# Kernel optimization log

Measured on AMD Instinct MI355X. Metric: run time of the kernel, lower is better.

The kernel has to match this reference:

```python
import jax, jax.numpy as jnp
import numpy as np
from jax import lax

LOW_T = 25.0    # int(0.1 * 255)
HIGH_T = 76.0   # int(0.3 * 255)
HYST_ITERS = 64 # cap on hysteresis propagation sweeps
TG22 = 0.4142135623730951  # tan(22.5 deg)
TG67 = 2.414213562373095   # tan(67.5 deg)

SOBEL_X = jnp.array([[-1., 0., 1.], [-2., 0., 2.], [-1., 0., 1.]], dtype=jnp.float32)
SOBEL_Y = jnp.array([[-1., -2., -1.], [0., 0., 0.], [1., 2., 1.]], dtype=jnp.float32)


def _conv3(x, k):
    # x: [B,H,W]; reflect-101 border like cv2.Sobel default
    xp = jnp.pad(x, ((0, 0), (1, 1), (1, 1)), mode='reflect')
    return lax.conv_general_dilated(xp[:, None], k[None, None], (1, 1), 'VALID')[:, 0]


def _dilate3x3(m):
    # 3x3 max-pool (8-connected dilation); m is nonnegative float 0/1
    return lax.reduce_window(m, jnp.float32(0.0), lax.max, (1, 3, 3), (1, 1, 1), 'SAME')


def canny_edge(image, low, high):
    """Batched Canny. image: [B,C,H,W] in [0,1] -> edges [B,1,H,W] in {0,1}."""
    image = lax.stop_gradient(image)  # mirrors .cpu().detach().numpy()
    B, C, H, W = image.shape
    if C == 3:
        gray = 0.299 * image[:, 0] + 0.587 * image[:, 1] + 0.114 * image[:, 2]
    else:
        gray = image[:, 0]
    # (img*255).astype(np.uint8) == floor toward zero for values in [0,1]
    g = jnp.clip(jnp.floor(gray * 255.0), 0.0, 255.0)

    gx = _conv3(g, SOBEL_X)
    gy = _conv3(g, SOBEL_Y)
    mag = jnp.abs(gx) + jnp.abs(gy)  # cv2 default L2gradient=False -> L1 magnitude

    # --- non-maximum suppression (OpenCV-style direction quantization) ---
    mp = jnp.pad(mag, ((0, 0), (1, 1), (1, 1)))

    def sh(dy, dx):
        return mp[:, 1 + dy:1 + dy + H, 1 + dx:1 + dx + W]

    ax, ay = jnp.abs(gx), jnp.abs(gy)
    horiz = ay <= TG22 * ax              # gradient ~horizontal: compare L/R
    vert = ay >= TG67 * ax               # gradient ~vertical: compare U/D
    diag = ~(horiz | vert)
    same_sign = (gx * gy) >= 0
    d1 = diag & same_sign                # 45 deg diagonal

    keep_h = (mag > sh(0, -1)) & (mag >= sh(0, 1))
    keep_v = (mag > sh(-1, 0)) & (mag >= sh(1, 0))
    keep_d1 = (mag > sh(-1, -1)) & (mag >= sh(1, 1))
    keep_d2 = (mag > sh(-1, 1)) & (mag >= sh(1, -1))
    keep = jnp.where(horiz, keep_h,
           jnp.where(vert, keep_v,
           jnp.where(d1, keep_d1, keep_d2)))
    nms = jnp.where(keep, mag, 0.0)

    # --- double threshold + hysteresis (iterative 8-connected propagation) ---
    weak = (nms > low).astype(jnp.float32)
    strong = (nms > high).astype(jnp.float32)

    def cond(state):
        cur, prev, i = state
        return jnp.logical_and(i < HYST_ITERS, jnp.any(cur != prev))

    def body(state):
        cur, prev, i = state
        new = jnp.minimum(_dilate3x3(cur), weak)          # grow strong into weak
        new = jnp.maximum(new, strong)
        return new, cur, i + 1

    edges, _, _ = lax.while_loop(cond, body, (strong, -jnp.ones_like(strong), 0))
    return edges[:, None]  # [B,1,H,W]


def reference(image_A, image_B):
    image_A = jnp.where(image_A.max() > 1, image_A / 2.0, image_A)
    image_B = jnp.where(image_B.max() > 1, image_B / 2.0, image_B)
    edges_A = canny_edge(image_A, LOW_T, HIGH_T)
    edges_B = canny_edge(image_B, LOW_T, HIGH_T)
    diff = edges_A - edges_B
    return jnp.sqrt(jnp.sum(diff * diff))  # Frobenius norm over all elements


def setup_inputs() -> dict:
    key = jax.random.key(0)
    kA, kB = jax.random.split(key)
    image_A = jax.random.uniform(kA, (32, 3, 512, 512), dtype=jnp.float32)
    image_B = jax.random.uniform(kB, (32, 3, 512, 512), dtype=jnp.float32)
    return {"image_A": image_A, "image_B": image_B}
```

## Files before the change

### kernel.cpp

```cpp
#include <hip/hip_runtime.h>
#include <cstdint>

#define IMG_H 512
#define IMG_W 512
#define WPR 8

typedef unsigned long long u64;

__global__ __launch_bounds__(256) void canny_nms_kernel(
    const float* __restrict__ imgA, const float* __restrict__ imgB,
    u64* __restrict__ strong_out, u64* __restrict__ weak_out)
{
    const int img = blockIdx.z;
    const int ty0 = blockIdx.y * 64;
    const int tx0 = blockIdx.x * 64;
    const float* src = (img < 32) ? imgA + (size_t)img * 3 * IMG_H * IMG_W
                                  : imgB + (size_t)(img - 32) * 3 * IMG_H * IMG_W;

    __shared__ _Float16 sg[68][68];
    __shared__ unsigned short su[66][66];
    const int tid = threadIdx.x;

    for (int idx = tid; idx < 68 * 68; idx += 256) {
        int ly = idx / 68, lx = idx - ly * 68;
        int iy = ty0 - 2 + ly, ix = tx0 - 2 + lx;
        iy = iy < 0 ? -iy : (iy > IMG_H - 1 ? 2 * (IMG_H - 1) - iy : iy);
        ix = ix < 0 ? -ix : (ix > IMG_W - 1 ? 2 * (IMG_W - 1) - ix : ix);
        size_t p = (size_t)iy * IMG_W + ix;
        float r   = src[p];
        float gch = src[(size_t)IMG_H * IMG_W + p];
        float b   = src[(size_t)2 * IMG_H * IMG_W + p];
        float gray = 0.299f * r + 0.587f * gch + 0.114f * b;
        sg[ly][lx] = (_Float16)fminf(fmaxf(floorf(gray * 255.0f), 0.0f), 255.0f);
    }
    __syncthreads();

    for (int idx = tid; idx < 66 * 66; idx += 256) {
        int ly = idx / 66, lx = idx - ly * 66;
        int iy = ty0 - 1 + ly, ix = tx0 - 1 + lx;
        unsigned short pack = 0;
        if ((unsigned)iy < (unsigned)IMG_H && (unsigned)ix < (unsigned)IMG_W) {
            int a = ly + 1, b = lx + 1;
            float tl = (float)sg[a-1][b-1], tc = (float)sg[a-1][b], tr = (float)sg[a-1][b+1];
            float ml = (float)sg[a][b-1],                           mr = (float)sg[a][b+1];
            float bl = (float)sg[a+1][b-1], bc = (float)sg[a+1][b], br = (float)sg[a+1][b+1];
            float gx = (tr + 2.0f*mr + br) - (tl + 2.0f*ml + bl);
            float gy = (bl + 2.0f*bc + br) - (tl + 2.0f*tc + tr);
            float ax = fabsf(gx), ay = fabsf(gy);
            int mag = (int)(ax + ay);
            bool horiz = ay <= 0.4142135623730951f * ax;
            bool vert  = ay >= 2.414213562373095f * ax;
            int dir = horiz ? 0 : (vert ? 1 : ((gx * gy >= 0.0f) ? 2 : 3));
            pack = (unsigned short)(mag | (dir << 12));
        }
        su[ly][lx] = pack;
    }
    __syncthreads();

    const int lane = tid & 63;
    const int wv = tid >> 6;
    for (int ry = wv; ry < 64; ry += 4) {
        int my = ry + 1, mx = lane + 1;
        int vc   = su[my][mx];
        int magc = vc & 0xFFF, dir = vc >> 12;
        int n_l  = su[my][mx-1]   & 0xFFF, n_r  = su[my][mx+1]   & 0xFFF;
        int n_t  = su[my-1][mx]   & 0xFFF, n_b  = su[my+1][mx]   & 0xFFF;
        int n_tl = su[my-1][mx-1] & 0xFFF, n_br = su[my+1][mx+1] & 0xFFF;
        int n_tr = su[my-1][mx+1] & 0xFFF, n_bl = su[my+1][mx-1] & 0xFFF;
        bool keep = (dir == 0) ? (magc > n_l  && magc >= n_r)
                  : (dir == 1) ? (magc > n_t  && magc >= n_b)
                  : (dir == 2) ? (magc > n_tl && magc >= n_br)
                               : (magc > n_tr && magc >= n_bl);
        int nms = keep ? magc : 0;
        u64 wweak   = __ballot(nms > 25);
        u64 wstrong = __ballot(nms > 76);
        if (lane == 0) {
            size_t o = ((size_t)img * IMG_H + (ty0 + ry)) * WPR + blockIdx.x;
            weak_out[o]   = wweak;
            strong_out[o] = wstrong;
        }
    }
}

__global__ __launch_bounds__(512) void hyst_diff_kernel(
    const u64* __restrict__ strong_in, const u64* __restrict__ weak_in,
    unsigned int* __restrict__ sum, unsigned int* __restrict__ done,
    float* __restrict__ out)
{
    const int pair = blockIdx.z;
    const int ty = blockIdx.y, tx = blockIdx.x;
    const int half = threadIdx.x >> 8;
    const int t = threadIdx.x & 255;
    const int img = pair + (half ? 32 : 0);

    __shared__ u64 sh[2][4][256];
    __shared__ int sflag;

    const int row0 = ty * 128 - 64;
    const int wc0  = tx * 2 - 1;
    const size_t ibase = (size_t)img * IMG_H * WPR;

    u64 c[4], wk[4];
    {
        int gr = row0 + t;
        bool rok = (gr >= 0 && gr < IMG_H);
        #pragma unroll
        for (int j = 0; j < 4; ++j) {
            int wc = wc0 + j;
            bool ok = rok && wc >= 0 && wc < WPR;
            size_t o = ibase + (size_t)gr * WPR + wc;
            c[j]  = ok ? strong_in[o] : 0ULL;
            wk[j] = ok ? weak_in[o]   : 0ULL;
        }
    }
    if (threadIdx.x == 0) sflag = 0;

    for (int it = 0; it < 64; ++it) {
        u64 h[4];
        h[0] = c[0] | (c[0] << 1) | (c[0] >> 1) | (c[1] << 63);
        h[1] = c[1] | (c[1] << 1) | (c[1] >> 1) | (c[0] >> 63) | (c[2] << 63);
        h[2] = c[2] | (c[2] << 1) | (c[2] >> 1) | (c[1] >> 63) | (c[3] << 63);
        h[3] = c[3] | (c[3] << 1) | (c[3] >> 1) | (c[2] >> 63);
        #pragma unroll
        for (int j = 0; j < 4; ++j) sh[half][j][t] = h[j];
        __syncthreads();

        u64 n[4] = {h[0], h[1], h[2], h[3]};
        if (t > 0) {
            #pragma unroll
            for (int j = 0; j < 4; ++j) n[j] |= sh[half][j][t - 1];
        }
        if (t < 255) {
            #pragma unroll
            for (int j = 0; j < 4; ++j) n[j] |= sh[half][j][t + 1];
        }
        #pragma unroll
        for (int j = 0; j < 4; ++j) n[j] &= wk[j];

        u64 delta = (n[0] ^ c[0]) | (n[1] ^ c[1]) | (n[2] ^ c[2]) | (n[3] ^ c[3]);
        if (delta) sflag = it + 1;
        __syncthreads();
        #pragma unroll
        for (int j = 0; j < 4; ++j) c[j] = n[j];
        if (sflag != it + 1) break;
    }

    sh[half][0][t] = c[1];
    sh[half][1][t] = c[2];
    __syncthreads();

    unsigned int v = 0;
    if (half == 0 && t >= 64 && t < 192) {
        v  = (unsigned int)__popcll(sh[0][0][t] ^ sh[1][0][t]);
        v += (unsigned int)__popcll(sh[0][1][t] ^ sh[1][1][t]);
    }
    #pragma unroll
    for (int off = 32; off > 0; off >>= 1) v += __shfl_down(v, off);
    if ((threadIdx.x & 63) == 0 && v != 0) atomicAdd(sum, v);
    __syncthreads();

    if (threadIdx.x == 0) {
        __threadfence();
        unsigned int ticket = atomicAdd(done, 1);
        if (ticket == 4 * 4 * 32 - 1) {
            __threadfence();
            unsigned int s = atomicAdd(sum, 0u);
            out[0] = sqrtf((float)s);
        }
    }
}

extern "C" void kernel_launch(void* const* d_in, const int* in_sizes, int n_in,
                              void* d_out, int out_size, void* d_ws, size_t ws_size,
                              hipStream_t stream) {
    const float* imgA = (const float*)d_in[0];
    const float* imgB = (const float*)d_in[1];
    float* out = (float*)d_out;
    char* ws = (char*)d_ws;
    u64* strong_m = (u64*)(ws);
    u64* weak_m   = (u64*)(ws + (2u << 20));
    unsigned int* counters = (unsigned int*)(ws + (4u << 20));

    hipMemsetAsync(counters, 0, 2 * sizeof(unsigned int), stream);

    dim3 g1(8, 8, 64);
    canny_nms_kernel<<<g1, 256, 0, stream>>>(imgA, imgB, strong_m, weak_m);

    dim3 g2(4, 4, 32);
    hyst_diff_kernel<<<g2, 512, 0, stream>>>(strong_m, weak_m,
                                             counters, counters + 1, out);
}
```

Baseline: 282.5 us.

## Stream rows per wavefront for Canny NMS and register-tile hysteresis

The Sobel/NMS kernel is rewritten so each wavefront streams down a 64-column strip of 32 rows. It keeps sliding row sums in registers and exchanges neighbours with lane shuffles, with no shared-memory tiles or block barriers, which removes the halo recompute and LDS traffic. The hysteresis kernel now gives each lane 4 rows in registers and exchanges boundaries by shuffle inside one wavefront per image, replacing the per-iteration block syncs with a ballot-based convergence check. In exchange the NMS grid has fewer, longer blocks with more register pressure, and the hysteresis grid has only 128-thread blocks, which lowers parallelism.

```diff
diff --git a/kernel.cpp b/kernel.cpp
--- a/kernel.cpp
+++ b/kernel.cpp
@@ -1,165 +1,184 @@
 #include <hip/hip_runtime.h>
 #include <cstdint>
 
-#define IMG_H 512
-#define IMG_W 512
-#define WPR 8
-
 typedef unsigned long long u64;
 
-__global__ __launch_bounds__(256) void canny_nms_kernel(
+__device__ __forceinline__ int reflect_row(int t) {
+    return t < 0 ? -t : (t > 511 ? 1022 - t : t);
+}
+
+__global__ __launch_bounds__(256, 6) void canny_stream(
     const float* __restrict__ imgA, const float* __restrict__ imgB,
     u64* __restrict__ strong_out, u64* __restrict__ weak_out)
 {
-    const int img = blockIdx.z;
-    const int ty0 = blockIdx.y * 64;
-    const int tx0 = blockIdx.x * 64;
-    const float* src = (img < 32) ? imgA + (size_t)img * 3 * IMG_H * IMG_W
-                                  : imgB + (size_t)(img - 32) * 3 * IMG_H * IMG_W;
-
-    __shared__ _Float16 sg[68][68];
-    __shared__ unsigned short su[66][66];
-    const int tid = threadIdx.x;
-
-    for (int idx = tid; idx < 68 * 68; idx += 256) {
-        int ly = idx / 68, lx = idx - ly * 68;
-        int iy = ty0 - 2 + ly, ix = tx0 - 2 + lx;
-        iy = iy < 0 ? -iy : (iy > IMG_H - 1 ? 2 * (IMG_H - 1) - iy : iy);
-        ix = ix < 0 ? -ix : (ix > IMG_W - 1 ? 2 * (IMG_W - 1) - ix : ix);
-        size_t p = (size_t)iy * IMG_W + ix;
-        float r   = src[p];
-        float gch = src[(size_t)IMG_H * IMG_W + p];
-        float b   = src[(size_t)2 * IMG_H * IMG_W + p];
-        float gray = 0.299f * r + 0.587f * gch + 0.114f * b;
-        sg[ly][lx] = (_Float16)fminf(fmaxf(floorf(gray * 255.0f), 0.0f), 255.0f);
-    }
-    __syncthreads();
-
-    for (int idx = tid; idx < 66 * 66; idx += 256) {
-        int ly = idx / 66, lx = idx - ly * 66;
-        int iy = ty0 - 1 + ly, ix = tx0 - 1 + lx;
-        unsigned short pack = 0;
-        if ((unsigned)iy < (unsigned)IMG_H && (unsigned)ix < (unsigned)IMG_W) {
-            int a = ly + 1, b = lx + 1;
-            float tl = (float)sg[a-1][b-1], tc = (float)sg[a-1][b], tr = (float)sg[a-1][b+1];
-            float ml = (float)sg[a][b-1],                           mr = (float)sg[a][b+1];
-            float bl = (float)sg[a+1][b-1], bc = (float)sg[a+1][b], br = (float)sg[a+1][b+1];
-            float gx = (tr + 2.0f*mr + br) - (tl + 2.0f*ml + bl);
-            float gy = (bl + 2.0f*bc + br) - (tl + 2.0f*tc + tr);
-            float ax = fabsf(gx), ay = fabsf(gy);
-            int mag = (int)(ax + ay);
+    const int img  = blockIdx.z;
+    const int lane = threadIdx.x & 63;
+    const int W    = blockIdx.x * 4 + (threadIdx.x >> 6);
+    const int col  = W * 64 + lane;
+    const int y0   = blockIdx.y * 32;
+    const float* src = (img < 32) ? imgA + (size_t)img * 786432
+                                  : imgB + (size_t)(img - 32) * 786432;
+    const bool leftEdge = (W == 0), rightEdge = (W == 7);
+    const bool lane0 = (lane == 0), lane63 = (lane == 63);
+    int hcol = (lane < 2) ? (W * 64 - 2 + lane)
+             : (lane >= 62) ? (W * 64 + 64 + (lane - 62)) : col;
+    hcol = min(max(hcol, 0), 511);
+
+    float s0=0,s1=0,s2=0,d0=0,d1=0,d2=0;
+    float sh0=0,sh1=0,sh2=0,dh0=0,dh1=0,dh2=0;
+    float m0=0,m1=0,m2=0,mh0=0,mh1=0,mh2=0;
+    float gx1=0,gy1=0,gx2=0,gy2=0;
+
+    int rr = reflect_row(y0 - 2);
+    const float* p = src + (size_t)rr * 512;
+    float pr = p[col],  pg = p[262144 + col],  pb = p[524288 + col];
+    float qr = p[hcol], qg = p[262144 + hcol], qb = p[524288 + hcol];
+
+    for (int t = y0 - 2; t <= y0 + 33; ++t) {
+        float cr=pr, cg=pg, cb=pb, hr=qr, hg=qg, hb=qb;
+        rr = reflect_row(t + 1);
+        p = src + (size_t)rr * 512;
+        pr = p[col];  pg = p[262144 + col];  pb = p[524288 + col];
+        qr = p[hcol]; qg = p[262144 + hcol]; qb = p[524288 + hcol];
+
+        float gv = fminf(fmaxf(floorf((0.299f*cr + 0.587f*cg + 0.114f*cb) * 255.0f), 0.0f), 255.0f);
+        float hv = fminf(fmaxf(floorf((0.299f*hr + 0.587f*hg + 0.114f*hb) * 255.0f), 0.0f), 255.0f);
+
+        float gl  = __shfl_up(gv, 1);
+        float grr = __shfl_down(gv, 1);
+        float h0  = __shfl(hv, 0),  h1  = __shfl(hv, 1);
+        float h62 = __shfl(hv, 62), h63 = __shfl(hv, 63);
+        if (lane0)  gl  = leftEdge  ? grr : h1;
+        if (lane63) grr = rightEdge ? gl  : h62;
+
+        s0=s1; s1=s2; d0=d1; d1=d2;
+        s2 = gl + 2.0f*gv + grr;  d2 = grr - gl;
+        sh0=sh1; sh1=sh2; dh0=dh1; dh1=dh2;
+        sh2 = lane0 ? (h0 + 2.0f*h1 + gv) : (gv + 2.0f*h62 + h63);
+        dh2 = lane0 ? (gv - h0)           : (h63 - gv);
+
+        float gx = d0 + 2.0f*d1 + d2;
+        float gy = s2 - s0;
+        float mnew = fabsf(gx) + fabsf(gy);
+        float gxh = dh0 + 2.0f*dh1 + dh2;
+        float gyh = sh2 - sh0;
+        float mhnew = fabsf(gxh) + fabsf(gyh);
+        bool rowOK = (unsigned)(t - 1) < 512u;
+        if (!rowOK) { mnew = 0.0f; mhnew = 0.0f; }
+        if ((lane0 && leftEdge) || (lane63 && rightEdge)) mhnew = 0.0f;
+        gx1 = gx2; gy1 = gy2; gx2 = gx; gy2 = gy;
+        m0=m1; m1=m2; m2=mnew;
+        mh0=mh1; mh1=mh2; mh2=mhnew;
+
+        if (t >= y0 + 2) {
+            float l0 = lane0  ? mh0 : __shfl_up(m0, 1);
+            float l1 = lane0  ? mh1 : __shfl_up(m1, 1);
+            float l2 = lane0  ? mh2 : __shfl_up(m2, 1);
+            float r0 = lane63 ? mh0 : __shfl_down(m0, 1);
+            float r1 = lane63 ? mh1 : __shfl_down(m1, 1);
+            float r2 = lane63 ? mh2 : __shfl_down(m2, 1);
+            float ax = fabsf(gx1), ay = fabsf(gy1);
             bool horiz = ay <= 0.4142135623730951f * ax;
             bool vert  = ay >= 2.414213562373095f * ax;
-            int dir = horiz ? 0 : (vert ? 1 : ((gx * gy >= 0.0f) ? 2 : 3));
-            pack = (unsigned short)(mag | (dir << 12));
-        }
-        su[ly][lx] = pack;
-    }
-    __syncthreads();
-
-    const int lane = tid & 63;
-    const int wv = tid >> 6;
-    for (int ry = wv; ry < 64; ry += 4) {
-        int my = ry + 1, mx = lane + 1;
-        int vc   = su[my][mx];
-        int magc = vc & 0xFFF, dir = vc >> 12;
-        int n_l  = su[my][mx-1]   & 0xFFF, n_r  = su[my][mx+1]   & 0xFFF;
-        int n_t  = su[my-1][mx]   & 0xFFF, n_b  = su[my+1][mx]   & 0xFFF;
-        int n_tl = su[my-1][mx-1] & 0xFFF, n_br = su[my+1][mx+1] & 0xFFF;
-        int n_tr = su[my-1][mx+1] & 0xFFF, n_bl = su[my+1][mx-1] & 0xFFF;
-        bool keep = (dir == 0) ? (magc > n_l  && magc >= n_r)
-                  : (dir == 1) ? (magc > n_t  && magc >= n_b)
-                  : (dir == 2) ? (magc > n_tl && magc >= n_br)
-                               : (magc > n_tr && magc >= n_bl);
-        int nms = keep ? magc : 0;
-        u64 wweak   = __ballot(nms > 25);
-        u64 wstrong = __ballot(nms > 76);
-        if (lane == 0) {
-            size_t o = ((size_t)img * IMG_H + (ty0 + ry)) * WPR + blockIdx.x;
-            weak_out[o]   = wweak;
-            strong_out[o] = wstrong;
-        }
-    }
-}
-
-__global__ __launch_bounds__(512) void hyst_diff_kernel(
+            bool dg1   = !(horiz || vert) && (gx1 * gy1 >= 0.0f);
+            bool keep = horiz ? (m1 > l1 && m1 >= r1)
+                      : vert  ? (m1 > m0 && m1 >= m2)
+                      : dg1   ? (m1 > l0 && m1 >= r2)
+                              : (m1 > r0 && m1 >= l2);
+            float nms = keep ? m1 : 0.0f;
+            u64 wweak   = __ballot(nms > 25.0f);
+            u64 wstrong = __ballot(nms > 76.0f);
+            if (lane0) {
+                size_t o = ((size_t)img * 512 + (t - 2)) * 8 + W;
+                weak_out[o]   = wweak;
+                strong_out[o] = wstrong;
+            }
+        }
+    }
+}
+
+__global__ __launch_bounds__(128) void hyst_diff_kernel(
     const u64* __restrict__ strong_in, const u64* __restrict__ weak_in,
     unsigned int* __restrict__ sum, unsigned int* __restrict__ done,
     float* __restrict__ out)
 {
     const int pair = blockIdx.z;
     const int ty = blockIdx.y, tx = blockIdx.x;
-    const int half = threadIdx.x >> 8;
-    const int t = threadIdx.x & 255;
+    const int half = threadIdx.x >> 6;
+    const int lane = threadIdx.x & 63;
     const int img = pair + (half ? 32 : 0);
 
-    __shared__ u64 sh[2][4][256];
-    __shared__ int sflag;
+    __shared__ u64 bint[128 * 2];
 
     const int row0 = ty * 128 - 64;
     const int wc0  = tx * 2 - 1;
-    const size_t ibase = (size_t)img * IMG_H * WPR;
-
-    u64 c[4], wk[4];
-    {
-        int gr = row0 + t;
-        bool rok = (gr >= 0 && gr < IMG_H);
+    const size_t ibase = (size_t)img * 512 * 8;
+
+    u64 c[4][4], wk[4][4];
+    #pragma unroll
+    for (int r = 0; r < 4; ++r) {
+        int gr = row0 + lane * 4 + r;
+        bool rok = (gr >= 0 && gr < 512);
         #pragma unroll
         for (int j = 0; j < 4; ++j) {
             int wc = wc0 + j;
-            bool ok = rok && wc >= 0 && wc < WPR;
-            size_t o = ibase + (size_t)gr * WPR + wc;
-            c[j]  = ok ? strong_in[o] : 0ULL;
-            wk[j] = ok ? weak_in[o]   : 0ULL;
-        }
-    }
-    if (threadIdx.x == 0) sflag = 0;
+            bool ok = rok && wc >= 0 && wc < 8;
+            size_t o = ibase + (size_t)gr * 8 + wc;
+            c[r][j]  = ok ? strong_in[o] : 0ULL;
+            wk[r][j] = ok ? weak_in[o]   : 0ULL;
+        }
+    }
 
     for (int it = 0; it < 64; ++it) {
-        u64 h[4];
-        h[0] = c[0] | (c[0] << 1) | (c[0] >> 1) | (c[1] << 63);
-        h[1] = c[1] | (c[1] << 1) | (c[1] >> 1) | (c[0] >> 63) | (c[2] << 63);
-        h[2] = c[2] | (c[2] << 1) | (c[2] >> 1) | (c[1] >> 63) | (c[3] << 63);
-        h[3] = c[3] | (c[3] << 1) | (c[3] >> 1) | (c[2] >> 63);
-        #pragma unroll
-        for (int j = 0; j < 4; ++j) sh[half][j][t] = h[j];
-        __syncthreads();
-
-        u64 n[4] = {h[0], h[1], h[2], h[3]};
-        if (t > 0) {
-            #pragma unroll
-            for (int j = 0; j < 4; ++j) n[j] |= sh[half][j][t - 1];
-        }
-        if (t < 255) {
-            #pragma unroll
-            for (int j = 0; j < 4; ++j) n[j] |= sh[half][j][t + 1];
-        }
-        #pragma unroll
-        for (int j = 0; j < 4; ++j) n[j] &= wk[j];
-
-        u64 delta = (n[0] ^ c[0]) | (n[1] ^ c[1]) | (n[2] ^ c[2]) | (n[3] ^ c[3]);
-        if (delta) sflag = it + 1;
-        __syncthreads();
-        #pragma unroll
-        for (int j = 0; j < 4; ++j) c[j] = n[j];
-        if (sflag != it + 1) break;
-    }
-
-    sh[half][0][t] = c[1];
-    sh[half][1][t] = c[2];
+        u64 h[4][4];
+        #pragma unroll
+        for (int r = 0; r < 4; ++r) {
+            h[r][0] = c[r][0] | (c[r][0] << 1) | (c[r][0] >> 1) | (c[r][1] << 63);
+            h[r][1] = c[r][1] | (c[r][1] << 1) | (c[r][1] >> 1) | (c[r][0] >> 63) | (c[r][2] << 63);
+            h[r][2] = c[r][2] | (c[r][2] << 1) | (c[r][2] >> 1) | (c[r][1] >> 63) | (c[r][3] << 63);
+            h[r][3] = c[r][3] | (c[r][3] << 1) | (c[r][3] >> 1) | (c[r][2] >> 63);
+        }
+        u64 delta = 0ULL;
+        #pragma unroll
+        for (int j = 0; j < 4; ++j) {
+            u64 top = __shfl_up(h[3][j], 1);
+            u64 bot = __shfl_down(h[0][j], 1);
+            if (lane == 0)  top = 0ULL;
+            if (lane == 63) bot = 0ULL;
+            u64 n0 = (h[0][j] | top     | h[1][j]) & wk[0][j];
+            u64 n1 = (h[1][j] | h[0][j] | h[2][j]) & wk[1][j];
+            u64 n2 = (h[2][j] | h[1][j] | h[3][j]) & wk[2][j];
+            u64 n3 = (h[3][j] | h[2][j] | bot    ) & wk[3][j];
+            delta |= (n0 ^ c[0][j]) | (n1 ^ c[1][j]) | (n2 ^ c[2][j]) | (n3 ^ c[3][j]);
+            c[0][j] = n0; c[1][j] = n1; c[2][j] = n2; c[3][j] = n3;
+        }
+        if (__ballot(delta != 0ULL) == 0ULL) break;
+    }
+
+    if (half == 1 && lane >= 16 && lane < 48) {
+        #pragma unroll
+        for (int r = 0; r < 4; ++r) {
+            int lr = lane * 4 + r - 64;
+            bint[lr * 2 + 0] = c[r][1];
+            bint[lr * 2 + 1] = c[r][2];
+        }
+    }
     __syncthreads();
 
     unsigned int v = 0;
-    if (half == 0 && t >= 64 && t < 192) {
-        v  = (unsigned int)__popcll(sh[0][0][t] ^ sh[1][0][t]);
-        v += (unsigned int)__popcll(sh[0][1][t] ^ sh[1][1][t]);
+    if (half == 0 && lane >= 16 && lane < 48) {
+        #pragma unroll
+        for (int r = 0; r < 4; ++r) {
+            int lr = lane * 4 + r - 64;
+            v += (unsigned int)__popcll(c[r][1] ^ bint[lr * 2 + 0]);
+            v += (unsigned int)__popcll(c[r][2] ^ bint[lr * 2 + 1]);
+        }
     }
     #pragma unroll
     for (int off = 32; off > 0; off >>= 1) v += __shfl_down(v, off);
-    if ((threadIdx.x & 63) == 0 && v != 0) atomicAdd(sum, v);
-    __syncthreads();
 
     if (threadIdx.x == 0) {
+        if (v != 0) atomicAdd(sum, v);
         __threadfence();
         unsigned int ticket = atomicAdd(done, 1);
         if (ticket == 4 * 4 * 32 - 1) {
@@ -183,10 +202,10 @@
 
     hipMemsetAsync(counters, 0, 2 * sizeof(unsigned int), stream);
 
-    dim3 g1(8, 8, 64);
-    canny_nms_kernel<<<g1, 256, 0, stream>>>(imgA, imgB, strong_m, weak_m);
+    dim3 g1(2, 16, 64);
+    canny_stream<<<g1, 256, 0, stream>>>(imgA, imgB, strong_m, weak_m);
 
     dim3 g2(4, 4, 32);
-    hyst_diff_kernel<<<g2, 512, 0, stream>>>(strong_m, weak_m,
+    hyst_diff_kernel<<<g2, 128, 0, stream>>>(strong_m, weak_m,
                                              counters, counters + 1, out);
 }
```

Measured after the change: 253.8 us. -10.2%, faster.
